# Kernel tuning notes

Measured on AMD Instinct MI355X. Metric: run time of the kernel, lower is better.

## Reference

```python
import jax, jax.numpy as jnp
import numpy as np

M, K, N = 1024, 8192, 8192
PACK = 16  # 16 two-bit codes per int32 word


def _pack_ternary(codes):
    # codes: (N, K) int32 with values in {0,1,3} -> (N, K//16) int32
    c = codes.reshape(N, K // PACK, PACK).astype(jnp.uint32)
    shifts = (jnp.arange(PACK, dtype=jnp.uint32) * 2)
    packed = jnp.sum(c << shifts, axis=-1, dtype=jnp.uint32)
    return jax.lax.bitcast_convert_type(packed, jnp.int32)


def setup_inputs() -> dict:
    key = jax.random.key(0)
    kx, kw, kb = jax.random.split(key, 3)
    x = jax.random.normal(kx, (M, K), dtype=jnp.float16)
    # ternary codes drawn from {0,1,3} (code 2 is unused by the format)
    vals = jnp.array([0, 1, 3], dtype=jnp.int32)
    codes = vals[jax.random.randint(kw, (N, K), 0, 3)]
    packed_w = _pack_ternary(codes)
    bias = jax.random.normal(kb, (N,), dtype=jnp.float16)
    return {"x": x, "packed_w": packed_w, "bias": bias}


def _unpack(packed_w):
    # (N, K//16) int32 -> (N, K) fp16 weights with values in {0,1,3}
    shifts = jnp.arange(PACK, dtype=jnp.int32) * 2
    w = (packed_w[:, :, None] >> shifts) & 3  # mask keeps low 2 bits even with arithmetic shift
    return w.reshape(packed_w.shape[0], -1).astype(jnp.float16)


def reference(x, packed_w, bias):
    w = _unpack(packed_w)  # (N, K)
    # Y = X W^T + b, fp32 accumulation as in the CUDA/Triton GEMM, fp16 output
    y = jnp.einsum('mk,nk->mn', x, w, preferred_element_type=jnp.float32)
    y = y.astype(jnp.float16) + bias
    return y
```

## Files before the change

### kernel.cpp

```cpp
#include <hip/hip_runtime.h>
#include <hip/hip_fp16.h>
#include <stdint.h>

#define M_DIM 1024
#define N_DIM 8192
#define K_DIM 8192
#define KP    (K_DIM / 16)

#define BM 128
#define BN 128
#define BK 64
#define NTHREADS 256
#define B_STRIDE 144
#define B_BUF    (BN * B_STRIDE)

#define MT_STRIDE 2097152
#define KT_STRIDE 16384

typedef _Float16 half8   __attribute__((ext_vector_type(8)));
typedef __fp16   fp16x2  __attribute__((ext_vector_type(2)));
typedef float    f32x4   __attribute__((ext_vector_type(4)));
typedef float    f32x16  __attribute__((ext_vector_type(16)));

__device__ __forceinline__ uint32_t cvt2(float a, float b) {
  fp16x2 p = __builtin_amdgcn_cvt_pkrtz(a, b);
  return __builtin_bit_cast(uint32_t, p);
}

__device__ __forceinline__ void unpack_word(uint32_t u, uint32_t out[8]) {
  const uint32_t T = 0x42063C00u;
  uint32_t U0 = u & 0x33333333u;
  uint32_t U1 = (u >> 2) & 0x33333333u;
#pragma unroll
  for (int b = 0; b < 4; ++b) {
    uint32_t lo2 = (U0 >> (8 * b)) & 0xFFu;
    uint32_t hi2 = (U1 >> (8 * b)) & 0xFFu;
    uint32_t sel = ((lo2 | (hi2 << 8)) * 0x1001u) & 0x03030303u;
    uint32_t P = __builtin_amdgcn_perm(0u, T, sel);
    out[2 * b]     = __builtin_amdgcn_perm(P, 0u, 0x05000400u);
    out[2 * b + 1] = __builtin_amdgcn_perm(P, 0u, 0x07000600u);
  }
}

__global__ __launch_bounds__(256)
void cvt_x_t(const float* __restrict__ x, char* __restrict__ xhT) {
  __shared__ __align__(16) char st[16384];
  const int b  = blockIdx.x;
  const int mt = b >> 7, kt = b & 127;
  const int t  = threadIdx.x;
#pragma unroll
  for (int p = 0; p < 8; ++p) {
    int f   = t + 256 * p;
    int R   = f >> 4;
    int cc4 = f & 15;
    float4 v = *(const float4*)(x + (size_t)(mt * 128 + R) * K_DIM + kt * 64 + cc4 * 4);
    uint32_t w0 = cvt2(v.x, v.y), w1 = cvt2(v.z, v.w);
    int c8 = cc4 >> 1, hh = cc4 & 1;
    int i32 = R >> 5, r = R & 31, ks = c8 >> 1, q = c8 & 1;
    *(uint2*)(st + i32 * 4096 + ks * 1024 + q * 512 + r * 16 + hh * 8) = make_uint2(w0, w1);
  }
  __syncthreads();
  char* outb = xhT + (size_t)mt * MT_STRIDE + (size_t)kt * KT_STRIDE;
#pragma unroll
  for (int e = 0; e < 4; ++e) {
    int d = (e * 256 + t) * 16;
    *(uint4*)(outb + d) = *(const uint4*)(st + d);
  }
}

__global__ __launch_bounds__(NTHREADS, 2)
void ternary_gemm_rA(const char* __restrict__ xhT,
                     const int*  __restrict__ pw,
                     const float* __restrict__ bias,
                     float*       __restrict__ out) {
  __shared__ __align__(16) char BsB[2 * B_BUF];

  const int tid  = threadIdx.x;
  const int lane = tid & 63;
  const int w    = tid >> 6;
  const int wm   = w >> 1, wn = w & 1;
  const int bid  = blockIdx.x;
  const int mt   = bid & 7;
  const int bm   = mt * BM;
  const int bn   = (bid >> 3) * BN;

  const char* pA[2];
#pragma unroll
  for (int i = 0; i < 2; ++i)
    pA[i] = xhT + (size_t)mt * MT_STRIDE + (wm * 2 + i) * 4096 + lane * 16;

  const int rT = tid >> 1, hT = tid & 1;
  const int2* gB = (const int2*)pw + (size_t)(bn + rT) * (KP / 2) + hT;
  int dBoff[4];
#pragma unroll
  for (int h = 0; h < 4; ++h) dBoff[h] = rT * B_STRIDE + (hT * 4 + h) * 16;

  int offB[2][4];
#pragma unroll
  for (int j = 0; j < 2; ++j)
#pragma unroll
    for (int ks = 0; ks < 4; ++ks)
      offB[j][ks] = (wn * 64 + j * 32 + (lane & 31)) * B_STRIDE + (ks * 2 + (lane >> 5)) * 16;

  f32x16 acc[2][2];
#pragma unroll
  for (int i = 0; i < 2; ++i)
#pragma unroll
    for (int j = 0; j < 2; ++j) acc[i][j] = (f32x16)(0.f);

  const int NT = K_DIM / BK;

  {
    int2 w0 = gB[0];
    uint32_t o0[8], o1[8];
    unpack_word((uint32_t)w0.x, o0);
    unpack_word((uint32_t)w0.y, o1);
    *(uint4*)(BsB + dBoff[0]) = make_uint4(o0[0], o0[1], o0[2], o0[3]);
    *(uint4*)(BsB + dBoff[1]) = make_uint4(o0[4], o0[5], o0[6], o0[7]);
    *(uint4*)(BsB + dBoff[2]) = make_uint4(o1[0], o1[1], o1[2], o1[3]);
    *(uint4*)(BsB + dBoff[3]) = make_uint4(o1[4], o1[5], o1[6], o1[7]);
  }
  half8 aCur[2][4], aNxt[2][4];
#pragma unroll
  for (int i = 0; i < 2; ++i)
#pragma unroll
    for (int ks = 0; ks < 4; ++ks)
      aCur[i][ks] = *(const half8*)(pA[i] + ks * 1024);
#pragma unroll
  for (int i = 0; i < 2; ++i) pA[i] += KT_STRIDE;
  int2 wcur = gB[2];
  __syncthreads();

  for (int kt = 0; kt < NT; ++kt) {
    const int cur = kt & 1;

#pragma unroll
    for (int i = 0; i < 2; ++i)
#pragma unroll
      for (int ks = 0; ks < 4; ++ks)
        aNxt[i][ks] = *(const half8*)(pA[i] + ks * 1024);
    if (kt < NT - 2) {
#pragma unroll
      for (int i = 0; i < 2; ++i) pA[i] += KT_STRIDE;
    }
    int kn2 = (kt + 2 < NT) ? (kt + 2) : (NT - 1);
    int2 wnxt = gB[kn2 * 2];

    const char* bb = BsB + cur * B_BUF;
#pragma unroll
    for (int ks = 0; ks < 4; ++ks) {
      half8 bf0 = *(const half8*)(bb + offB[0][ks]);
      half8 bf1 = *(const half8*)(bb + offB[1][ks]);
      acc[0][0] = __builtin_amdgcn_mfma_f32_32x32x16_f16(aCur[0][ks], bf0, acc[0][0], 0, 0, 0);
      acc[0][1] = __builtin_amdgcn_mfma_f32_32x32x16_f16(aCur[0][ks], bf1, acc[0][1], 0, 0, 0);
      acc[1][0] = __builtin_amdgcn_mfma_f32_32x32x16_f16(aCur[1][ks], bf0, acc[1][0], 0, 0, 0);
      acc[1][1] = __builtin_amdgcn_mfma_f32_32x32x16_f16(aCur[1][ks], bf1, acc[1][1], 0, 0, 0);
    }

    {
      char* wb = BsB + (cur ^ 1) * B_BUF;
      uint32_t o0[8], o1[8];
      unpack_word((uint32_t)wcur.x, o0);
      unpack_word((uint32_t)wcur.y, o1);
      *(uint4*)(wb + dBoff[0]) = make_uint4(o0[0], o0[1], o0[2], o0[3]);
      *(uint4*)(wb + dBoff[1]) = make_uint4(o0[4], o0[5], o0[6], o0[7]);
      *(uint4*)(wb + dBoff[2]) = make_uint4(o1[0], o1[1], o1[2], o1[3]);
      *(uint4*)(wb + dBoff[3]) = make_uint4(o1[4], o1[5], o1[6], o1[7]);
    }

    __syncthreads();
    wcur = wnxt;
#pragma unroll
    for (int i = 0; i < 2; ++i)
#pragma unroll
      for (int ks = 0; ks < 4; ++ks) aCur[i][ks] = aNxt[i][ks];
  }

#pragma unroll
  for (int j = 0; j < 2; ++j) {
    int n = bn + wn * 64 + j * 32 + (lane & 31);
    __half hb = __float2half_rn(bias[n]);
#pragma unroll
    for (int i = 0; i < 2; ++i) {
      int mbase = bm + wm * 64 + i * 32 + 4 * (lane >> 5);
#pragma unroll
      for (int reg = 0; reg < 16; ++reg) {
        int m = mbase + (reg & 3) + 8 * (reg >> 2);
        __half hy = __float2half_rn(acc[i][j][reg]);
        out[(size_t)m * N_DIM + n] = __half2float(__hadd(hy, hb));
      }
    }
  }
}

__device__ __forceinline__ uint32_t unpack_pair16(uint32_t u, int p) {
  uint32_t c0 = (u >> (4 * p)) & 3u;
  uint32_t c1 = (u >> (4 * p + 2)) & 3u;
  uint32_t lo = (c0 & 1u) * 0x3C00u + (c0 >> 1) * 0x0600u;
  uint32_t hi = (c1 & 1u) * 0x3C00u + (c1 >> 1) * 0x0600u;
  return lo | (hi << 16);
}

__global__ __launch_bounds__(NTHREADS, 2)
void ternary_gemm(const float* __restrict__ x,
                  const int*   __restrict__ pw,
                  const float* __restrict__ bias,
                  float*       __restrict__ out) {
  __shared__ __align__(16) char AsB[128 * B_STRIDE];
  __shared__ __align__(16) char BsB[128 * B_STRIDE];

  const int tid  = threadIdx.x;
  const int lane = tid & 63;
  const int w    = tid >> 6;
  const int wm   = w >> 1, wn = w & 1;
  const int bid  = blockIdx.x;
  const int bm   = (bid & 7) * 128;
  const int bn   = (bid >> 3) * 128;

  const int rT = tid >> 1, hT = tid & 1;
  const float* gA = x + (size_t)(bm + rT) * K_DIM + hT * 32;
  char* const  lA = AsB + rT * B_STRIDE + hT * 64;
  const int2* gB = (const int2*)pw + (size_t)(bn + rT) * (KP / 2) + hT;
  char* dBp[4];
#pragma unroll
  for (int h = 0; h < 4; ++h)
    dBp[h] = BsB + rT * B_STRIDE + (hT * 4 + h) * 16;

  int offA[4][2], offB[4][2];
#pragma unroll
  for (int i = 0; i < 4; ++i)
#pragma unroll
    for (int ks = 0; ks < 2; ++ks) {
      int c = ks * 4 + (lane >> 4);
      offA[i][ks] = (wm * 64 + i * 16 + (lane & 15)) * B_STRIDE + c * 16;
      offB[i][ks] = (wn * 64 + i * 16 + (lane & 15)) * B_STRIDE + c * 16;
    }

  f32x4 acc[4][4];
#pragma unroll
  for (int i = 0; i < 4; ++i)
#pragma unroll
    for (int j = 0; j < 4; ++j)
      acc[i][j] = (f32x4){0.f, 0.f, 0.f, 0.f};

  const int NT = K_DIM / BK;
  for (int kt = 0; kt < NT; ++kt) {
    __syncthreads();
    int2 wcur = gB[kt * 2];
    float4 av[8];
#pragma unroll
    for (int v = 0; v < 8; ++v) av[v] = *(const float4*)(gA + kt * BK + v * 4);
    uint32_t d0[8], d1[8];
#pragma unroll
    for (int p = 0; p < 8; ++p) d0[p] = unpack_pair16((uint32_t)wcur.x, p);
#pragma unroll
    for (int p = 0; p < 8; ++p) d1[p] = unpack_pair16((uint32_t)wcur.y, p);
    *(uint4*)dBp[0] = make_uint4(d0[0], d0[1], d0[2], d0[3]);
    *(uint4*)dBp[1] = make_uint4(d0[4], d0[5], d0[6], d0[7]);
    *(uint4*)dBp[2] = make_uint4(d1[0], d1[1], d1[2], d1[3]);
    *(uint4*)dBp[3] = make_uint4(d1[4], d1[5], d1[6], d1[7]);
#pragma unroll
    for (int v = 0; v < 4; ++v) {
      uint4 aw;
      aw.x = cvt2(av[2 * v].x, av[2 * v].y);
      aw.y = cvt2(av[2 * v].z, av[2 * v].w);
      aw.z = cvt2(av[2 * v + 1].x, av[2 * v + 1].y);
      aw.w = cvt2(av[2 * v + 1].z, av[2 * v + 1].w);
      *(uint4*)(lA + v * 16) = aw;
    }
    __syncthreads();
#pragma unroll
    for (int ks = 0; ks < 2; ++ks) {
      half8 af[4], bf[4];
#pragma unroll
      for (int i = 0; i < 4; ++i) af[i] = *(const half8*)(AsB + offA[i][ks]);
#pragma unroll
      for (int j = 0; j < 4; ++j) bf[j] = *(const half8*)(BsB + offB[j][ks]);
#pragma unroll
      for (int i = 0; i < 4; ++i)
#pragma unroll
        for (int j = 0; j < 4; ++j)
          acc[i][j] = __builtin_amdgcn_mfma_f32_16x16x32_f16(af[i], bf[j], acc[i][j], 0, 0, 0);
    }
  }
#pragma unroll
  for (int j = 0; j < 4; ++j) {
    int n = bn + wn * 64 + j * 16 + (lane & 15);
    __half hb = __float2half_rn(bias[n]);
#pragma unroll
    for (int i = 0; i < 4; ++i) {
      int m0 = bm + wm * 64 + i * 16 + (lane >> 4) * 4;
#pragma unroll
      for (int r = 0; r < 4; ++r) {
        __half hy = __float2half_rn(acc[i][j][r]);
        out[(size_t)(m0 + r) * N_DIM + n] = __half2float(__hadd(hy, hb));
      }
    }
  }
}

extern "C" void kernel_launch(void* const* d_in, const int* in_sizes, int n_in,
                              void* d_out, int out_size, void* d_ws, size_t ws_size,
                              hipStream_t stream) {
  (void)in_sizes; (void)n_in; (void)out_size;
  const float* x    = (const float*)d_in[0];
  const int*   pwp  = (const int*)d_in[1];
  const float* bias = (const float*)d_in[2];
  float*       outp = (float*)d_out;

  const size_t need = (size_t)M_DIM * K_DIM * 2;
  if (ws_size >= need) {
    char* xhT = (char*)d_ws;
    cvt_x_t<<<8 * 128, 256, 0, stream>>>(x, xhT);
    dim3 grid((M_DIM / BM) * (N_DIM / BN));
    ternary_gemm_rA<<<grid, NTHREADS, 0, stream>>>(xhT, pwp, bias, outp);
  } else {
    dim3 grid((M_DIM / 128) * (N_DIM / 128));
    ternary_gemm<<<grid, NTHREADS, 0, stream>>>(x, pwp, bias, outp);
  }
}
```

Measured before the change: 239.3 us.

## Stage packed ternary words in LDS and decode B fragments in registers

Instead of unpacking the ternary weights to fp16 in shared memory (128x144-byte tiles, double buffered), the kernel now stores only the packed int32 words in a small 4 KB LDS stage. Each wave reads its row's packed words and decodes its MFMA B fragments in registers just before use. The main loop is also unrolled by two with ping-pong A register buffers, which removes the per-iteration register copy. This cuts LDS footprint and traffic and could allow higher occupancy. The cost is that every wave (wm=0 and wm=1) decodes the same B fragments, duplicating ALU work that now sits in the MFMA critical path.

Result: no change. 237.0 us (-0.9%).

```diff
diff --git a/kernel.cpp b/kernel.cpp
--- a/kernel.cpp
+++ b/kernel.cpp
@@ -12,7 +12,6 @@
 #define BK 64
 #define NTHREADS 256
 #define B_STRIDE 144
-#define B_BUF    (BN * B_STRIDE)
 
 #define MT_STRIDE 2097152
 #define KT_STRIDE 16384
@@ -27,19 +26,22 @@
   return __builtin_bit_cast(uint32_t, p);
 }
 
-__device__ __forceinline__ void unpack_word(uint32_t u, uint32_t out[8]) {
+__device__ __forceinline__ half8 dec_frag(uint32_t word, uint32_t sh) {
   const uint32_t T = 0x42063C00u;
-  uint32_t U0 = u & 0x33333333u;
-  uint32_t U1 = (u >> 2) & 0x33333333u;
-#pragma unroll
-  for (int b = 0; b < 4; ++b) {
-    uint32_t lo2 = (U0 >> (8 * b)) & 0xFFu;
-    uint32_t hi2 = (U1 >> (8 * b)) & 0xFFu;
-    uint32_t sel = ((lo2 | (hi2 << 8)) * 0x1001u) & 0x03030303u;
-    uint32_t P = __builtin_amdgcn_perm(0u, T, sel);
-    out[2 * b]     = __builtin_amdgcn_perm(P, 0u, 0x05000400u);
-    out[2 * b + 1] = __builtin_amdgcn_perm(P, 0u, 0x07000600u);
-  }
+  uint32_t h  = (word >> sh) & 0xFFFFu;
+  uint32_t W  = (h & 0x3333u) | ((h << 14) & 0x33330000u);
+  uint32_t c0 = __builtin_amdgcn_perm(0u, W, 0x04040200u);
+  uint32_t c1 = __builtin_amdgcn_perm(0u, W, 0x04040301u);
+  uint32_t s0 = (c0 * 0x1001u) & 0x03030303u;
+  uint32_t s1 = (c1 * 0x1001u) & 0x03030303u;
+  uint32_t P0 = __builtin_amdgcn_perm(0u, T, s0);
+  uint32_t P1 = __builtin_amdgcn_perm(0u, T, s1);
+  uint4 v;
+  v.x = __builtin_amdgcn_perm(P0, 0u, 0x05000400u);
+  v.y = __builtin_amdgcn_perm(P0, 0u, 0x07000600u);
+  v.z = __builtin_amdgcn_perm(P1, 0u, 0x05000400u);
+  v.w = __builtin_amdgcn_perm(P1, 0u, 0x07000600u);
+  return __builtin_bit_cast(half8, v);
 }
 
 __global__ __launch_bounds__(256)
@@ -69,11 +71,11 @@
 }
 
 __global__ __launch_bounds__(NTHREADS, 2)
-void ternary_gemm_rA(const char* __restrict__ xhT,
+void ternary_gemm_dc(const char* __restrict__ xhT,
                      const int*  __restrict__ pw,
                      const float* __restrict__ bias,
                      float*       __restrict__ out) {
-  __shared__ __align__(16) char BsB[2 * B_BUF];
+  __shared__ __align__(16) char stg[2 * 2048];
 
   const int tid  = threadIdx.x;
   const int lane = tid & 63;
@@ -91,54 +93,40 @@
 
   const int rT = tid >> 1, hT = tid & 1;
   const int2* gB = (const int2*)pw + (size_t)(bn + rT) * (KP / 2) + hT;
-  int dBoff[4];
-#pragma unroll
-  for (int h = 0; h < 4; ++h) dBoff[h] = rT * B_STRIDE + (hT * 4 + h) * 16;
-
-  int offB[2][4];
+  const int stOff = rT * 16 + hT * 8;
+
+  int rowOff[2];
 #pragma unroll
   for (int j = 0; j < 2; ++j)
+    rowOff[j] = (wn * 64 + j * 32 + (lane & 31)) * 16;
+  const uint32_t sh = (lane >> 5) * 16;
+
+  f32x16 acc[2][2];
+#pragma unroll
+  for (int i = 0; i < 2; ++i)
+#pragma unroll
+    for (int j = 0; j < 2; ++j) acc[i][j] = (f32x16)(0.f);
+
+  const int NT = K_DIM / BK;
+
+  *(int2*)(stg + stOff) = gB[0];
+  half8 aA[2][4], aB[2][4];
+#pragma unroll
+  for (int i = 0; i < 2; ++i)
 #pragma unroll
     for (int ks = 0; ks < 4; ++ks)
-      offB[j][ks] = (wn * 64 + j * 32 + (lane & 31)) * B_STRIDE + (ks * 2 + (lane >> 5)) * 16;
-
-  f32x16 acc[2][2];
-#pragma unroll
-  for (int i = 0; i < 2; ++i)
-#pragma unroll
-    for (int j = 0; j < 2; ++j) acc[i][j] = (f32x16)(0.f);
-
-  const int NT = K_DIM / BK;
-
-  {
-    int2 w0 = gB[0];
-    uint32_t o0[8], o1[8];
-    unpack_word((uint32_t)w0.x, o0);
-    unpack_word((uint32_t)w0.y, o1);
-    *(uint4*)(BsB + dBoff[0]) = make_uint4(o0[0], o0[1], o0[2], o0[3]);
-    *(uint4*)(BsB + dBoff[1]) = make_uint4(o0[4], o0[5], o0[6], o0[7]);
-    *(uint4*)(BsB + dBoff[2]) = make_uint4(o1[0], o1[1], o1[2], o1[3]);
-    *(uint4*)(BsB + dBoff[3]) = make_uint4(o1[4], o1[5], o1[6], o1[7]);
-  }
-  half8 aCur[2][4], aNxt[2][4];
-#pragma unroll
-  for (int i = 0; i < 2; ++i)
-#pragma unroll
-    for (int ks = 0; ks < 4; ++ks)
-      aCur[i][ks] = *(const half8*)(pA[i] + ks * 1024);
+      aA[i][ks] = *(const half8*)(pA[i] + ks * 1024);
 #pragma unroll
   for (int i = 0; i < 2; ++i) pA[i] += KT_STRIDE;
   int2 wcur = gB[2];
   __syncthreads();
 
-  for (int kt = 0; kt < NT; ++kt) {
-    const int cur = kt & 1;
-
+  auto step = [&](half8 (&aC)[2][4], half8 (&aN)[2][4], int cur, int kt) {
 #pragma unroll
     for (int i = 0; i < 2; ++i)
 #pragma unroll
       for (int ks = 0; ks < 4; ++ks)
-        aNxt[i][ks] = *(const half8*)(pA[i] + ks * 1024);
+        aN[i][ks] = *(const half8*)(pA[i] + ks * 1024);
     if (kt < NT - 2) {
 #pragma unroll
       for (int i = 0; i < 2; ++i) pA[i] += KT_STRIDE;
@@ -146,34 +134,28 @@
     int kn2 = (kt + 2 < NT) ? (kt + 2) : (NT - 1);
     int2 wnxt = gB[kn2 * 2];
 
-    const char* bb = BsB + cur * B_BUF;
+    uint32_t wr0[4], wr1[4];
+    *(uint4*)wr0 = *(const uint4*)(stg + cur * 2048 + rowOff[0]);
+    *(uint4*)wr1 = *(const uint4*)(stg + cur * 2048 + rowOff[1]);
+    *(int2*)(stg + (cur ^ 1) * 2048 + stOff) = wcur;
+
 #pragma unroll
     for (int ks = 0; ks < 4; ++ks) {
-      half8 bf0 = *(const half8*)(bb + offB[0][ks]);
-      half8 bf1 = *(const half8*)(bb + offB[1][ks]);
-      acc[0][0] = __builtin_amdgcn_mfma_f32_32x32x16_f16(aCur[0][ks], bf0, acc[0][0], 0, 0, 0);
-      acc[0][1] = __builtin_amdgcn_mfma_f32_32x32x16_f16(aCur[0][ks], bf1, acc[0][1], 0, 0, 0);
-      acc[1][0] = __builtin_amdgcn_mfma_f32_32x32x16_f16(aCur[1][ks], bf0, acc[1][0], 0, 0, 0);
-      acc[1][1] = __builtin_amdgcn_mfma_f32_32x32x16_f16(aCur[1][ks], bf1, acc[1][1], 0, 0, 0);
-    }
-
-    {
-      char* wb = BsB + (cur ^ 1) * B_BUF;
-      uint32_t o0[8], o1[8];
-      unpack_word((uint32_t)wcur.x, o0);
-      unpack_word((uint32_t)wcur.y, o1);
-      *(uint4*)(wb + dBoff[0]) = make_uint4(o0[0], o0[1], o0[2], o0[3]);
-      *(uint4*)(wb + dBoff[1]) = make_uint4(o0[4], o0[5], o0[6], o0[7]);
-      *(uint4*)(wb + dBoff[2]) = make_uint4(o1[0], o1[1], o1[2], o1[3]);
-      *(uint4*)(wb + dBoff[3]) = make_uint4(o1[4], o1[5], o1[6], o1[7]);
+      half8 bf0 = dec_frag(wr0[ks], sh);
+      half8 bf1 = dec_frag(wr1[ks], sh);
+      acc[0][0] = __builtin_amdgcn_mfma_f32_32x32x16_f16(aC[0][ks], bf0, acc[0][0], 0, 0, 0);
+      acc[0][1] = __builtin_amdgcn_mfma_f32_32x32x16_f16(aC[0][ks], bf1, acc[0][1], 0, 0, 0);
+      acc[1][0] = __builtin_amdgcn_mfma_f32_32x32x16_f16(aC[1][ks], bf0, acc[1][0], 0, 0, 0);
+      acc[1][1] = __builtin_amdgcn_mfma_f32_32x32x16_f16(aC[1][ks], bf1, acc[1][1], 0, 0, 0);
     }
 
     __syncthreads();
     wcur = wnxt;
-#pragma unroll
-    for (int i = 0; i < 2; ++i)
-#pragma unroll
-      for (int ks = 0; ks < 4; ++ks) aCur[i][ks] = aNxt[i][ks];
+  };
+
+  for (int kt = 0; kt < NT; kt += 2) {
+    step(aA, aB, 0, kt);
+    step(aB, aA, 1, kt + 1);
   }
 
 #pragma unroll
@@ -313,7 +295,7 @@
     char* xhT = (char*)d_ws;
     cvt_x_t<<<8 * 128, 256, 0, stream>>>(x, xhT);
     dim3 grid((M_DIM / BM) * (N_DIM / BN));
-    ternary_gemm_rA<<<grid, NTHREADS, 0, stream>>>(xhT, pwp, bias, outp);
+    ternary_gemm_dc<<<grid, NTHREADS, 0, stream>>>(xhT, pwp, bias, outp);
   } else {
     dim3 grid((M_DIM / 128) * (N_DIM / 128));
     ternary_gemm<<<grid, NTHREADS, 0, stream>>>(x, pwp, bias, outp);
```
